# Kernel tuning notes

Measured on AMD Instinct MI355X. Metric: run time of the kernel, lower is better.

## Reference

```python
import jax, jax.numpy as jnp
import numpy as np

H, D = 4, 32  # num_heads, per-head out dim (out_feats=128)
N_AGENT, N_GT, N_UAV = 50000, 50000, 50000
E = 600000
IN = 64


def _gat(x_src, x_dst, src, dst, W_src, W_dst, al, ar, W_res, b, num_dst):
    """DGL-style bipartite GATConv with residual, bias and ReLU activation."""
    fs = (x_src @ W_src).reshape(-1, H, D)      # [Ns,H,D]
    fd = (x_dst @ W_dst).reshape(-1, H, D)      # [Nd,H,D]
    el = jnp.sum(fs * al, axis=-1)              # [Ns,H]
    er = jnp.sum(fd * ar, axis=-1)              # [Nd,H]
    e = jax.nn.leaky_relu(el[src] + er[dst], 0.2)          # [E,H]
    # segment softmax over incoming edges of each dst node
    emax = jax.ops.segment_max(e, dst, num_segments=num_dst)   # [Nd,H], -inf for deg-0
    ee = jnp.exp(e - emax[dst])
    denom = jax.ops.segment_sum(ee, dst, num_segments=num_dst)
    a = ee / denom[dst]                          # [E,H]
    msg = fs[src] * a[:, :, None]                # [E,H,D]
    rst = jax.ops.segment_sum(msg, dst, num_segments=num_dst)  # [Nd,H,D]; zeros for deg-0
    res = (x_dst @ W_res).reshape(-1, H, D)      # residual projection
    out = jax.nn.relu(rst + res + b.reshape(1, H, D))
    return out.reshape(num_dst, H * D)


def setup_inputs() -> dict:
    key = jax.random.key(0)
    ks = jax.random.split(key, 20)
    s = 0.1  # weight init scale
    return {
        'x_gt': jax.random.normal(ks[0], (N_GT, IN), jnp.float32),
        'x_uav': jax.random.normal(ks[1], (N_UAV, IN), jnp.float32),
        'x_agent': jax.random.normal(ks[2], (N_AGENT, IN), jnp.float32),
        'src_gt': jax.random.randint(ks[3], (E,), 0, N_GT, jnp.int32),
        'dst_gt': jax.random.randint(ks[4], (E,), 0, N_AGENT, jnp.int32),
        'src_uav': jax.random.randint(ks[5], (E,), 0, N_UAV, jnp.int32),
        'dst_uav': jax.random.randint(ks[6], (E,), 0, N_AGENT, jnp.int32),
        'W_src_gt': s * jax.random.normal(ks[7], (IN, H * D), jnp.float32),
        'W_dst_gt': s * jax.random.normal(ks[8], (IN, H * D), jnp.float32),
        'attn_l_gt': s * jax.random.normal(ks[9], (H, D), jnp.float32),
        'attn_r_gt': s * jax.random.normal(ks[10], (H, D), jnp.float32),
        'W_res_gt': s * jax.random.normal(ks[11], (IN, H * D), jnp.float32),
        'b_gt': jnp.zeros((H * D,), jnp.float32),
        'W_src_uav': s * jax.random.normal(ks[12], (IN, H * D), jnp.float32),
        'W_dst_uav': s * jax.random.normal(ks[13], (IN, H * D), jnp.float32),
        'attn_l_uav': s * jax.random.normal(ks[14], (H, D), jnp.float32),
        'attn_r_uav': s * jax.random.normal(ks[15], (H, D), jnp.float32),
        'W_res_uav': s * jax.random.normal(ks[16], (IN, H * D), jnp.float32),
        'b_uav': jnp.zeros((H * D,), jnp.float32),
        'W_f': s * jax.random.normal(ks[17], (2 * H * D, H * D), jnp.float32),
        'b_f': jnp.zeros((H * D,), jnp.float32),
    }


def reference(x_gt, x_uav, x_agent, src_gt, dst_gt, src_uav, dst_uav,
              W_src_gt, W_dst_gt, attn_l_gt, attn_r_gt, W_res_gt, b_gt,
              W_src_uav, W_dst_uav, attn_l_uav, attn_r_uav, W_res_uav, b_uav,
              W_f, b_f):
    h_gt = _gat(x_gt, x_agent, src_gt, dst_gt, W_src_gt, W_dst_gt,
                attn_l_gt, attn_r_gt, W_res_gt, b_gt, N_AGENT)
    h_uav = _gat(x_uav, x_agent, src_uav, dst_uav, W_src_uav, W_dst_uav,
                 attn_l_uav, attn_r_uav, W_res_uav, b_uav, N_AGENT)
    h = jnp.concatenate([h_gt, h_uav], axis=1)   # [N_agent, 256]
    return jax.nn.relu(h @ W_f + b_f)            # [N_agent, 128]
```

## Files before the change

kernel.cpp:

```cpp
#include <hip/hip_runtime.h>
#include <hip/hip_bf16.h>

using bf16 = __hip_bfloat16;

#define NA 50000
#define NE 600000

#define NCH 96
#define CHE 12500
#define HROW 100032
#define PBINS 33344

typedef __attribute__((ext_vector_type(8))) short short8;
typedef __attribute__((ext_vector_type(4))) float f32x4;

#define HBUF_B   0u
#define FS_B     25600000u
#define EL_B     51200000u
#define RECS_B   54400000u
#define HIST_B   68800000u
#define ROW_B    78403072u
#define TOPS_B   78803076u
#define FLAG_B   78803588u
#define WST_GT_B 78803600u
#define WST_UAV_B 78819984u
#define WRT_B    78836368u
#define WFT_B    78869136u
#define ELT_GT_B 78934672u
#define ELT_UAV_B 78936720u
#define ERT_B    78938768u
#define RANK8_B  78940816u
#define WS_BYTES 80140816u

__device__ __forceinline__ float b2f(bf16 v) { return __bfloat162float(v); }

__device__ __forceinline__ float ldf(const void* p, size_t i, int f32) {
    return f32 ? ((const float*)p)[i] : b2f(((const bf16*)p)[i]);
}

__device__ __forceinline__ unsigned short f2bs(float v) {
    bf16 t = __float2bfloat16(v);
    return *(unsigned short*)&t;
}

__device__ __forceinline__ float lrelu_exp(float v) {
    v = v > 0.f ? v : 0.2f * v;
    return __expf(v);
}

__device__ __forceinline__ unsigned int pack_bf16x2(float a, float b) {
    return (unsigned int)f2bs(a) | ((unsigned int)f2bs(b) << 16);
}

__device__ __forceinline__ float lo_f(unsigned int u) { return __uint_as_float(u << 16); }
__device__ __forceinline__ float hi_f(unsigned int u) { return __uint_as_float(u & 0xffff0000u); }

__device__ __forceinline__ short8 ldfrag8(const void* p, size_t off, int f32) {
    if (!f32) return *(const short8*)((const unsigned short*)p + off);
    union { short8 s; unsigned int u[4]; } r;
    const float* fp = (const float*)p + off;
#pragma unroll
    for (int j = 0; j < 4; ++j) r.u[j] = pack_bf16x2(fp[2 * j], fp[2 * j + 1]);
    return r.s;
}

__device__ int probe_f32(const void* x0) {
    __shared__ int cnt;
    if (threadIdx.x == 0) cnt = 0;
    __syncthreads();
    const bf16* p = (const bf16*)x0;
    int bad = 0;
    for (int i = threadIdx.x; i < 1024; i += 256) {
        float av = fabsf(b2f(p[i]));
        if (!(av <= 1e6f)) bad++;
    }
    if (bad) atomicAdd(&cnt, bad);
    __syncthreads();
    return cnt > 8;
}

__global__ void HeteroVisionConv_29703993819529_kernel(
    const void* x0,
    const void* Wsg, const void* alg, const void* Wdg, const void* arg_,
    const void* Wsu, const void* alu, const void* Wdu, const void* aru,
    const void* Wrg, const void* Wru, const void* Wf,
    unsigned short* wsT_gt, unsigned short* wsT_uav, unsigned short* wrT,
    unsigned short* wfT, unsigned short* elT_gt, unsigned short* elT_uav,
    unsigned short* erT,
    int* flag, unsigned int* outp, long sent) {
    int b = blockIdx.x, t = threadIdx.x;
    int f32 = probe_f32(x0);
    if (b == 20) {
        if (t == 0) { flag[0] = f32; outp[sent] = 0x447A447Au; }
        return;
    }
    if (b < 8) {
        for (int i = t; i < 16 * 256; i += 256) {
            int n = b * 16 + (i >> 8), k = i & 255;
            wfT[n * 256 + k] = f2bs(ldf(Wf, (size_t)k * 128 + n, f32));
        }
    } else if (b < 12) {
        for (int i = t; i < 64 * 64; i += 256) {
            int n = (b - 8) * 64 + (i >> 6), k = i & 63;
            float v = (n < 128) ? ldf(Wrg, (size_t)k * 128 + n, f32)
                                : ldf(Wru, (size_t)k * 128 + (n - 128), f32);
            wrT[n * 64 + k] = f2bs(v);
        }
    } else if (b < 14) {
        for (int i = t; i < 64 * 64; i += 256) {
            int n = (b - 12) * 64 + (i >> 6), k = i & 63;
            wsT_gt[n * 64 + k] = f2bs(ldf(Wsg, (size_t)k * 128 + n, f32));
        }
    } else if (b < 16) {
        for (int i = t; i < 64 * 64; i += 256) {
            int n = (b - 14) * 64 + (i >> 6), k = i & 63;
            wsT_uav[n * 64 + k] = f2bs(ldf(Wsu, (size_t)k * 128 + n, f32));
        }
    } else {
        int m = b - 16;
        const void* Wm = (m == 0) ? Wsg : (m == 1) ? Wdg : (m == 2) ? Wsu : Wdu;
        const void* Am = (m == 0) ? alg : (m == 1) ? arg_ : (m == 2) ? alu : aru;
        int k = t >> 2, h = t & 3;
        float a = 0.f;
        for (int d = 0; d < 32; ++d)
            a += ldf(Wm, (size_t)k * 128 + h * 32 + d, f32) *
                 ldf(Am, (size_t)h * 32 + d, f32);
        unsigned short v = f2bs(a);
        if (m == 0) {
            elT_gt[h * 64 + k] = v;
            for (int i = t; i < 12 * 64; i += 256) elT_gt[(4 + (i >> 6)) * 64 + (i & 63)] = 0;
        } else if (m == 2) {
            elT_uav[h * 64 + k] = v;
            for (int i = t; i < 12 * 64; i += 256) elT_uav[(4 + (i >> 6)) * 64 + (i & 63)] = 0;
        } else if (m == 1) {
            erT[h * 64 + k] = v;
        } else {
            erT[(4 + h) * 64 + k] = v;
            for (int i = t; i < 8 * 64; i += 256) erT[(8 + (i >> 6)) * 64 + (i & 63)] = 0;
        }
    }
}

__global__ void fused_k(const int* dg, const int* du,
                        unsigned char* hist, unsigned char* rank8,
                        const void* xg, const void* xu, const void* xa,
                        const unsigned short* wsT_gt, const unsigned short* wsT_uav,
                        const unsigned short* elT_gt, const unsigned short* elT_uav,
                        const unsigned short* wrT, const unsigned short* erT,
                        const void* bg, const void* bu,
                        float* elbase, bf16* fs, bf16* hbuf, const int* flag) {
    __shared__ unsigned short Bt[256 * 72];
    __shared__ float bl[256];
    int b = blockIdx.x, t = threadIdx.x;

    if (b < NCH) {
        int c = b;
        int g = c >= 48;
        int eoff = (c - g * 48) * CHE;
        const int* dp = (g ? du : dg) + eoff;
        unsigned char* rk = rank8 + (size_t)g * NE + eoff;
        unsigned int* h32 = (unsigned int*)Bt;
        for (int p = 0; p < 3; ++p) {
            int binLo = p * PBINS;
            unsigned int* out = (unsigned int*)(hist + (size_t)c * HROW + binLo);
            bool live = (binLo + PBINS > g * NA) && (binLo < g * NA + NA);
            if (!live) {
                for (int i = t; i < PBINS / 4; i += 256) out[i] = 0u;
                continue;
            }
            for (int i = t; i < PBINS / 4; i += 256) h32[i] = 0u;
            __syncthreads();
            for (int i = t; i < CHE / 4; i += 256) {
                int4 d4 = *(const int4*)(dp + i * 4);
                int dd[4] = {d4.x, d4.y, d4.z, d4.w};
#pragma unroll
                for (int k = 0; k < 4; ++k) {
                    int rel = g * NA + dd[k] - binLo;
                    if (rel >= 0 && rel < PBINS) {
                        unsigned int sh8 = 8u * (rel & 3);
                        unsigned int old = atomicAdd(&h32[rel >> 2], 1u << sh8);
                        rk[i * 4 + k] = (unsigned char)((old >> sh8) & 255u);
                    }
                }
            }
            __syncthreads();
            for (int i = t; i < PBINS / 4; i += 256) out[i] = h32[i];
            __syncthreads();
        }
        return;
    }
    int nidx = b - NCH;
    int f32 = *flag;
    int lane = t & 63, w = t >> 6;
    int m = lane & 15, quad = lane >> 4;

    if (nidx < 1564) {
        int g = nidx / 782, bb = nidx % 782;
        const void* A = g ? xu : xg;
        const unsigned short* WT = g ? wsT_uav : wsT_gt;
        const unsigned short* ET = g ? elT_uav : elT_gt;
        float* elout = elbase + (g ? 400000 : 0);
        bf16* out = fs + (size_t)g * NA * 128;
        for (int i = t * 8; i < 128 * 64; i += 256 * 8) {
            short8 v = *(const short8*)(WT + i);
            int n = i >> 6, k = i & 63;
            *(short8*)&Bt[n * 72 + k] = v;
        }
        __syncthreads();
        int row = bb * 64 + w * 16 + m;
        int rowc = row < NA ? row : NA - 1;
        short8 a0 = ldfrag8(A, (size_t)rowc * 64 + quad * 8, f32);
        short8 a1 = ldfrag8(A, (size_t)rowc * 64 + 32 + quad * 8, f32);
        f32x4 acc[8];
#pragma unroll
        for (int nt = 0; nt < 8; ++nt) acc[nt] = (f32x4){0.f, 0.f, 0.f, 0.f};
#pragma unroll
        for (int nt = 0; nt < 8; ++nt) {
            short8 b0 = *(const short8*)&Bt[(nt * 16 + m) * 72 + quad * 8];
            short8 b1 = *(const short8*)&Bt[(nt * 16 + m) * 72 + 32 + quad * 8];
            acc[nt] = __builtin_amdgcn_mfma_f32_16x16x32_bf16(a0, b0, acc[nt], 0, 0, 0);
            acc[nt] = __builtin_amdgcn_mfma_f32_16x16x32_bf16(a1, b1, acc[nt], 0, 0, 0);
        }
        f32x4 eacc = (f32x4){0.f, 0.f, 0.f, 0.f};
        {
            short8 e0 = *(const short8*)&ET[m * 64 + quad * 8];
            short8 e1 = *(const short8*)&ET[m * 64 + 32 + quad * 8];
            eacc = __builtin_amdgcn_mfma_f32_16x16x32_bf16(a0, e0, eacc, 0, 0, 0);
            eacc = __builtin_amdgcn_mfma_f32_16x16x32_bf16(a1, e1, eacc, 0, 0, 0);
        }
        int srow = bb * 64 + w * 16 + quad * 4;
#pragma unroll
        for (int nt = 0; nt < 8; ++nt) {
#pragma unroll
            for (int r = 0; r < 4; ++r) {
                int rr = srow + r;
                if (rr < NA) out[(size_t)rr * 128 + nt * 16 + m] = __float2bfloat16(acc[nt][r]);
            }
        }
        if (m < 4) {
#pragma unroll
            for (int r = 0; r < 4; ++r) {
                int rr = srow + r;
                if (rr < NA) elout[(size_t)rr * 4 + m] = eacc[r];
            }
        }
        return;
    }
    int bb = nidx - 1564;
    for (int i = t * 8; i < 256 * 64; i += 256 * 8) {
        short8 v = *(const short8*)(wrT + i);
        int n = i >> 6, k = i & 63;
        *(short8*)&Bt[n * 72 + k] = v;
    }
    bl[t] = (t < 128) ? ldf(bg, t, f32) : ldf(bu, t - 128, f32);
    __syncthreads();
    int row = bb * 64 + w * 16 + m;
    int rowc = row < NA ? row : NA - 1;
    short8 a0 = ldfrag8(xa, (size_t)rowc * 64 + quad * 8, f32);
    short8 a1 = ldfrag8(xa, (size_t)rowc * 64 + 32 + quad * 8, f32);
    f32x4 acc[16];
#pragma unroll
    for (int nt = 0; nt < 16; ++nt) acc[nt] = (f32x4){0.f, 0.f, 0.f, 0.f};
#pragma unroll
    for (int nt = 0; nt < 16; ++nt) {
        short8 b0 = *(const short8*)&Bt[(nt * 16 + m) * 72 + quad * 8];
        short8 b1 = *(const short8*)&Bt[(nt * 16 + m) * 72 + 32 + quad * 8];
        acc[nt] = __builtin_amdgcn_mfma_f32_16x16x32_bf16(a0, b0, acc[nt], 0, 0, 0);
        acc[nt] = __builtin_amdgcn_mfma_f32_16x16x32_bf16(a1, b1, acc[nt], 0, 0, 0);
    }
    f32x4 eacc = (f32x4){0.f, 0.f, 0.f, 0.f};
    {
        short8 e0 = *(const short8*)&erT[m * 64 + quad * 8];
        short8 e1 = *(const short8*)&erT[m * 64 + 32 + quad * 8];
        eacc = __builtin_amdgcn_mfma_f32_16x16x32_bf16(a0, e0, eacc, 0, 0, 0);
        eacc = __builtin_amdgcn_mfma_f32_16x16x32_bf16(a1, e1, eacc, 0, 0, 0);
    }
    int srow = bb * 64 + w * 16 + quad * 4;
#pragma unroll
    for (int nt = 0; nt < 16; ++nt) {
        int col = nt * 16 + m;
#pragma unroll
        for (int r = 0; r < 4; ++r) {
            int rr = srow + r;
            if (rr < NA)
                hbuf[(size_t)rr * 256 + col] = __float2bfloat16(acc[nt][r] + bl[col]);
        }
    }
    if (m < 8) {
        float* ero = (m < 4) ? (elbase + 200000) : (elbase + 600000);
        int mm = m & 3;
#pragma unroll
        for (int r = 0; r < 4; ++r) {
            int rr = srow + r;
            if (rr < NA) ero[(size_t)rr * 4 + mm] = eacc[r];
        }
    }
}

__global__ void scan1_k(unsigned char* hist, unsigned int* row, unsigned int* tops) {
    __shared__ unsigned char ch[NCH * 1024];
    __shared__ unsigned int sh[256];
    int b = blockIdx.x, t = threadIdx.x;
    int base = b * 1024;
    int off = base + t * 4;
    for (int c = 0; c < NCH; ++c) {
        unsigned int w = 0u;
        if (off + 4 <= HROW) w = *(const unsigned int*)(hist + (size_t)c * HROW + off);
        *(unsigned int*)&ch[c * 1024 + t * 4] = w;
    }
    __syncthreads();
    unsigned int v[4];
    for (int j = 0; j < 4; ++j) {
        int idx = t * 4 + j;
        unsigned int run = 0;
        for (int c = 0; c < NCH; ++c) {
            unsigned int x = ch[c * 1024 + idx];
            ch[c * 1024 + idx] = (unsigned char)run;
            run += x;
        }
        v[j] = (base + idx < 100000) ? run : 0u;
    }
    __syncthreads();
    for (int c = 0; c < NCH; ++c) {
        if (off + 4 <= HROW)
            *(unsigned int*)(hist + (size_t)c * HROW + off) =
                *(const unsigned int*)&ch[c * 1024 + t * 4];
    }
    unsigned int s = v[0] + v[1] + v[2] + v[3];
    sh[t] = s;
    __syncthreads();
    for (int o = 1; o < 256; o <<= 1) {
        unsigned int x = (t >= o) ? sh[t - o] : 0u;
        __syncthreads();
        sh[t] += x;
        __syncthreads();
    }
    unsigned int run = sh[t] - s;
    for (int j = 0; j < 4; ++j) {
        if (base + j + t * 4 < 100000) row[base + t * 4 + j] = run;
        run += v[j];
    }
    if (t == 255) tops[b] = sh[255];
}

__global__ void scan2_k(unsigned int* tops, unsigned int* row) {
    __shared__ unsigned int sh[128];
    int t = threadIdx.x;
    unsigned int v = (t < 98) ? tops[t] : 0u;
    sh[t] = v;
    __syncthreads();
    for (int off = 1; off < 128; off <<= 1) {
        unsigned int x = (t >= off) ? sh[t - off] : 0u;
        __syncthreads();
        sh[t] += x;
        __syncthreads();
    }
    if (t < 98) tops[t] = sh[t] - v;
    if (t == 97) row[100000] = sh[97];
}

__global__ void scan3_k(unsigned int* row, const unsigned int* tops) {
    int b = blockIdx.x, t = threadIdx.x;
    unsigned int off = tops[b];
    for (int i = b * 1024 + t; i < b * 1024 + 1024; i += 256) {
        if (i < 100000) row[i] += off;
    }
}

__global__ void scatter_k(const int* sg, const int* dg, const int* su, const int* du,
                          const float* elbase, const unsigned int* row,
                          const unsigned char* hist, const unsigned char* rank8,
                          unsigned int* recs) {
    int idx = blockIdx.x * 256 + threadIdx.x;
    if (idx >= 2 * NE) return;
    int g = idx >= NE;
    int e = idx - g * NE;
    int s = (g ? su : sg)[e];
    int d = (g ? du : dg)[e];
    int c = g * 48 + e / CHE;
    int bin = g * NA + d;
    const float4* el4 = (const float4*)(elbase + (g ? 400000 : 0));
    const float4* er4 = (const float4*)(elbase + (g ? 600000 : 200000));
    unsigned int lr = rank8[idx];
    unsigned int cb = hist[(size_t)c * HROW + bin];
    unsigned int pos = row[bin] + cb + lr;
    float4 l = el4[s], r = er4[d];
    uint3 rec;
    rec.x = (unsigned int)s;
    rec.y = pack_bf16x2(lrelu_exp(l.x + r.x), lrelu_exp(l.y + r.y));
    rec.z = pack_bf16x2(lrelu_exp(l.z + r.z), lrelu_exp(l.w + r.w));
    *(uint3*)(recs + (size_t)pos * 3) = rec;
}

__global__ void gather_k(const unsigned int* row, const unsigned int* recs,
                         const bf16* fs, bf16* hbuf) {
    int wid = (blockIdx.x * 256 + threadIdx.x) >> 6;
    int lane = threadIdx.x & 63;
    if (wid >= 2 * NA) return;
    int g = wid / NA, d = wid - g * NA;
    int eg = lane >> 4;
    int cl = lane & 15;
    int hsel = cl >> 3;
    int hodd = (cl >> 2) & 1;
    unsigned int start = row[g * NA + d];
    unsigned int end   = row[g * NA + d + 1];
    const uint4* fs4 = (const uint4*)(fs + (size_t)g * NA * 128);

    float denom = 0.f;
    float a[8];
#pragma unroll
    for (int k = 0; k < 8; ++k) a[k] = 0.f;

    if (start < end) {
        uint3 rr[4], rn[4];
#pragma unroll
        for (int j = 0; j < 4; ++j) {
            unsigned int idx = start + 4 * j + eg;
            rr[j] = *(const uint3*)(recs + (size_t)(idx < end ? idx : end - 1) * 3);
        }
        for (unsigned int i = start; i < end; i += 16) {
            uint4 uu[4];
#pragma unroll
            for (int j = 0; j < 4; ++j) uu[j] = fs4[(size_t)rr[j].x * 16 + cl];
            unsigned int inext = i + 16;
#pragma unroll
            for (int j = 0; j < 4; ++j) {
                unsigned int idx = inext + 4 * j + eg;
                rn[j] = *(const uint3*)(recs + (size_t)(idx < end ? idx : end - 1) * 3);
            }
#pragma unroll
            for (int j = 0; j < 4; ++j) {
                unsigned int idx = i + 4 * j + eg;
                unsigned int pp = hsel ? rr[j].z : rr[j].y;
                float e = hodd ? hi_f(pp) : lo_f(pp);
                if (idx >= end) e = 0.f;
                denom += e;
                a[0] += lo_f(uu[j].x) * e;
                a[1] += hi_f(uu[j].x) * e;
                a[2] += lo_f(uu[j].y) * e;
                a[3] += hi_f(uu[j].y) * e;
                a[4] += lo_f(uu[j].z) * e;
                a[5] += hi_f(uu[j].z) * e;
                a[6] += lo_f(uu[j].w) * e;
                a[7] += hi_f(uu[j].w) * e;
            }
#pragma unroll
            for (int j = 0; j < 4; ++j) rr[j] = rn[j];
        }
    }
#pragma unroll
    for (int k = 0; k < 8; ++k) {
        a[k] += __shfl_xor(a[k], 16, 64);
        a[k] += __shfl_xor(a[k], 32, 64);
    }
    denom += __shfl_xor(denom, 16, 64);
    denom += __shfl_xor(denom, 32, 64);
    if (lane < 16) {
        float inv = (end > start) ? 1.f / denom : 0.f;
        uint4* hp = (uint4*)(hbuf + (size_t)d * 256 + g * 128) + cl;
        uint4 rv = *hp;
        float v0 = a[0] * inv + lo_f(rv.x);
        float v1 = a[1] * inv + hi_f(rv.x);
        float v2 = a[2] * inv + lo_f(rv.y);
        float v3 = a[3] * inv + hi_f(rv.y);
        float v4 = a[4] * inv + lo_f(rv.z);
        float v5 = a[5] * inv + hi_f(rv.z);
        float v6 = a[6] * inv + lo_f(rv.w);
        float v7 = a[7] * inv + hi_f(rv.w);
        v0 = v0 > 0.f ? v0 : 0.f;
        v1 = v1 > 0.f ? v1 : 0.f;
        v2 = v2 > 0.f ? v2 : 0.f;
        v3 = v3 > 0.f ? v3 : 0.f;
        v4 = v4 > 0.f ? v4 : 0.f;
        v5 = v5 > 0.f ? v5 : 0.f;
        v6 = v6 > 0.f ? v6 : 0.f;
        v7 = v7 > 0.f ? v7 : 0.f;
        uint4 o;
        o.x = pack_bf16x2(v0, v1);
        o.y = pack_bf16x2(v2, v3);
        o.z = pack_bf16x2(v4, v5);
        o.w = pack_bf16x2(v6, v7);
        *hp = o;
    }
}

__global__ void final_k(const bf16* hbuf, const unsigned short* wfT,
                        const void* bfp, void* outp, const int* flag) {
    int f32 = *flag;
    int b = blockIdx.x;
    __shared__ unsigned short Bt[128 * 72];
    __shared__ float bl[128];
    int t = threadIdx.x;
    if (t < 128) bl[t] = ldf(bfp, t, f32);
    int lane = t & 63, w = t >> 6;
    int m = lane & 15, quad = lane >> 4;
    int row = b * 64 + w * 16 + m;
    int rowc = row < NA ? row : NA - 1;
    f32x4 acc[8];
#pragma unroll
    for (int nt = 0; nt < 8; ++nt) acc[nt] = (f32x4){0.f, 0.f, 0.f, 0.f};
    for (int kc = 0; kc < 4; ++kc) {
        __syncthreads();
        for (int i = t * 8; i < 128 * 64; i += 256 * 8) {
            int n = i >> 6, k = i & 63;
            short8 v = *(const short8*)(wfT + (size_t)n * 256 + kc * 64 + k);
            *(short8*)&Bt[n * 72 + k] = v;
        }
        __syncthreads();
        short8 a0 = *(const short8*)((const unsigned short*)hbuf +
                                     (size_t)rowc * 256 + kc * 64 + quad * 8);
        short8 a1 = *(const short8*)((const unsigned short*)hbuf +
                                     (size_t)rowc * 256 + kc * 64 + 32 + quad * 8);
#pragma unroll
        for (int nt = 0; nt < 8; ++nt) {
            short8 b0 = *(const short8*)&Bt[(nt * 16 + m) * 72 + quad * 8];
            short8 b1 = *(const short8*)&Bt[(nt * 16 + m) * 72 + 32 + quad * 8];
            acc[nt] = __builtin_amdgcn_mfma_f32_16x16x32_bf16(a0, b0, acc[nt], 0, 0, 0);
            acc[nt] = __builtin_amdgcn_mfma_f32_16x16x32_bf16(a1, b1, acc[nt], 0, 0, 0);
        }
    }
    int srow = b * 64 + w * 16 + quad * 4;
#pragma unroll
    for (int nt = 0; nt < 8; ++nt) {
        int col = nt * 16 + m;
        float bv = bl[col];
#pragma unroll
        for (int r = 0; r < 4; ++r) {
            int rr = srow + r;
            if (rr < NA) {
                float v = acc[nt][r] + bv;
                v = v > 0.f ? v : 0.f;
                if (f32) ((float*)outp)[(size_t)rr * 128 + col] = v;
                else ((bf16*)outp)[(size_t)rr * 128 + col] = __float2bfloat16(v);
            }
        }
    }
}

extern "C" void kernel_launch(void* const* d_in, const int* in_sizes, int n_in,
                              void* d_out, int out_size, void* d_ws, size_t ws_size,
                              hipStream_t stream) {
    const void* x_gt     = d_in[0];
    const void* x_uav    = d_in[1];
    const void* x_ag     = d_in[2];
    const int*  src_gt   = (const int*)d_in[3];
    const int*  dst_gt   = (const int*)d_in[4];
    const int*  src_uav  = (const int*)d_in[5];
    const int*  dst_uav  = (const int*)d_in[6];
    const void* Wsrc_gt  = d_in[7];
    const void* Wdst_gt  = d_in[8];
    const void* al_gt    = d_in[9];
    const void* ar_gt    = d_in[10];
    const void* Wres_gt  = d_in[11];
    const void* b_gt     = d_in[12];
    const void* Wsrc_uav = d_in[13];
    const void* Wdst_uav = d_in[14];
    const void* al_uav   = d_in[15];
    const void* ar_uav   = d_in[16];
    const void* Wres_uav = d_in[17];
    const void* b_uav    = d_in[18];
    const void* W_f      = d_in[19];
    const void* b_f      = d_in[20];

    char* wsb = (char*)d_ws;
    bf16* hbuf = (bf16*)(wsb + HBUF_B);
    bf16* fs = (bf16*)(wsb + FS_B);
    float* el = (float*)(wsb + EL_B);
    unsigned int* recs = (unsigned int*)(wsb + RECS_B);
    unsigned char* hist = (unsigned char*)(wsb + HIST_B);
    unsigned int* row = (unsigned int*)(wsb + ROW_B);
    unsigned int* tops = (unsigned int*)(wsb + TOPS_B);
    int* flag = (int*)(wsb + FLAG_B);
    unsigned short* wsT_gt = (unsigned short*)(wsb + WST_GT_B);
    unsigned short* wsT_uav = (unsigned short*)(wsb + WST_UAV_B);
    unsigned short* wrT = (unsigned short*)(wsb + WRT_B);
    unsigned short* wfT = (unsigned short*)(wsb + WFT_B);
    unsigned short* elT_gt = (unsigned short*)(wsb + ELT_GT_B);
    unsigned short* elT_uav = (unsigned short*)(wsb + ELT_UAV_B);
    unsigned short* erT = (unsigned short*)(wsb + ERT_B);
    unsigned char* rank8 = (unsigned char*)(wsb + RANK8_B);

    if (ws_size < (size_t)WS_BYTES) {
        hipMemsetAsync(d_out, 0x42, (size_t)out_size * 2, stream);
        return;
    }

    long sent = (long)out_size / 2 - 1;

    HeteroVisionConv_29703993819529_kernel<<<21, 256, 0, stream>>>(
        x_gt, Wsrc_gt, al_gt, Wdst_gt, ar_gt, Wsrc_uav, al_uav, Wdst_uav, ar_uav,
        Wres_gt, Wres_uav, W_f,
        wsT_gt, wsT_uav, wrT, wfT, elT_gt, elT_uav, erT,
        flag, (unsigned int*)d_out, sent);
    fused_k<<<NCH + 2346, 256, 0, stream>>>(dst_gt, dst_uav, hist, rank8,
                                            x_gt, x_uav, x_ag,
                                            wsT_gt, wsT_uav, elT_gt, elT_uav,
                                            wrT, erT, b_gt, b_uav,
                                            el, fs, hbuf, flag);
    scan1_k<<<98, 256, 0, stream>>>(hist, row, tops);
    scan2_k<<<1, 128, 0, stream>>>(tops, row);
    scan3_k<<<98, 256, 0, stream>>>(row, tops);
    scatter_k<<<4688, 256, 0, stream>>>(src_gt, dst_gt, src_uav, dst_uav,
                                        el, row, hist, rank8, recs);
    gather_k<<<25000, 256, 0, stream>>>(row, recs, fs, hbuf);
    final_k<<<782, 256, 0, stream>>>(hbuf, wfT, b_f, d_out, flag);
}
```

Before: 302.2 us.

## Fold scan passes into last-block decoupled scan and pipeline gather loop

The three-kernel prefix scan becomes one kernel. The last block to finish, found with an atomic ticket counter, scans the per-block totals, and consumers add the block offset on read instead of running a separate fixup pass. This removes two kernel launches and a full pass over the row array. The gather loop is also restructured from 16-edge batches with 4 records per lane to a 4-edge-per-step software pipeline that prefetches two records ahead, and bf16 extraction now uses a shift instead of a select. The trade-offs are an extra tops load per scatter and per gather, and a different memory-level parallelism profile in gather.

```diff
diff --git a/kernel.cpp b/kernel.cpp
--- a/kernel.cpp
+++ b/kernel.cpp
@@ -86,12 +86,12 @@
     const void* Wrg, const void* Wru, const void* Wf,
     unsigned short* wsT_gt, unsigned short* wsT_uav, unsigned short* wrT,
     unsigned short* wfT, unsigned short* elT_gt, unsigned short* elT_uav,
-    unsigned short* erT,
+    unsigned short* erT, unsigned int* tops,
     int* flag, unsigned int* outp, long sent) {
     int b = blockIdx.x, t = threadIdx.x;
     int f32 = probe_f32(x0);
     if (b == 20) {
-        if (t == 0) { flag[0] = f32; outp[sent] = 0x447A447Au; }
+        if (t == 0) { flag[0] = f32; tops[120] = 0u; outp[sent] = 0x447A447Au; }
         return;
     }
     if (b < 8) {
@@ -300,6 +300,7 @@
 __global__ void scan1_k(unsigned char* hist, unsigned int* row, unsigned int* tops) {
     __shared__ unsigned char ch[NCH * 1024];
     __shared__ unsigned int sh[256];
+    __shared__ int lastf;
     int b = blockIdx.x, t = threadIdx.x;
     int base = b * 1024;
     int off = base + t * 4;
@@ -337,38 +338,37 @@
     }
     unsigned int run = sh[t] - s;
     for (int j = 0; j < 4; ++j) {
-        if (base + j + t * 4 < 100000) row[base + t * 4 + j] = run;
+        if (base + t * 4 + j < 100000) row[base + t * 4 + j] = run;
         run += v[j];
     }
     if (t == 255) tops[b] = sh[255];
-}
-
-__global__ void scan2_k(unsigned int* tops, unsigned int* row) {
-    __shared__ unsigned int sh[128];
-    int t = threadIdx.x;
-    unsigned int v = (t < 98) ? tops[t] : 0u;
-    sh[t] = v;
-    __syncthreads();
-    for (int off = 1; off < 128; off <<= 1) {
-        unsigned int x = (t >= off) ? sh[t - off] : 0u;
+    __threadfence();
+    __syncthreads();
+    if (t == 0) {
+        unsigned int tk = atomicAdd(&tops[120], 1u);
+        lastf = (tk == 97u);
+    }
+    __syncthreads();
+    if (!lastf) return;
+    unsigned int tv = (t < 98) ? __hip_atomic_load(&tops[t], __ATOMIC_RELAXED,
+                                                   __HIP_MEMORY_SCOPE_AGENT)
+                               : 0u;
+    __syncthreads();
+    sh[t] = tv;
+    __syncthreads();
+    for (int o = 1; o < 256; o <<= 1) {
+        unsigned int x = (t >= o) ? sh[t - o] : 0u;
         __syncthreads();
         sh[t] += x;
         __syncthreads();
     }
-    if (t < 98) tops[t] = sh[t] - v;
-    if (t == 97) row[100000] = sh[97];
-}
-
-__global__ void scan3_k(unsigned int* row, const unsigned int* tops) {
-    int b = blockIdx.x, t = threadIdx.x;
-    unsigned int off = tops[b];
-    for (int i = b * 1024 + t; i < b * 1024 + 1024; i += 256) {
-        if (i < 100000) row[i] += off;
-    }
+    if (t < 98) tops[t] = sh[t] - tv;
+    if (t == 97) row[100000] = tv;
 }
 
 __global__ void scatter_k(const int* sg, const int* dg, const int* su, const int* du,
                           const float* elbase, const unsigned int* row,
+                          const unsigned int* tops,
                           const unsigned char* hist, const unsigned char* rank8,
                           unsigned int* recs) {
     int idx = blockIdx.x * 256 + threadIdx.x;
@@ -383,7 +383,7 @@
     const float4* er4 = (const float4*)(elbase + (g ? 600000 : 200000));
     unsigned int lr = rank8[idx];
     unsigned int cb = hist[(size_t)c * HROW + bin];
-    unsigned int pos = row[bin] + cb + lr;
+    unsigned int pos = row[bin] + tops[bin >> 10] + cb + lr;
     float4 l = el4[s], r = er4[d];
     uint3 rec;
     rec.x = (unsigned int)s;
@@ -392,18 +392,20 @@
     *(uint3*)(recs + (size_t)pos * 3) = rec;
 }
 
-__global__ void gather_k(const unsigned int* row, const unsigned int* recs,
+__global__ void gather_k(const unsigned int* row, const unsigned int* tops,
+                         const unsigned int* recs,
                          const bf16* fs, bf16* hbuf) {
     int wid = (blockIdx.x * 256 + threadIdx.x) >> 6;
     int lane = threadIdx.x & 63;
     if (wid >= 2 * NA) return;
     int g = wid / NA, d = wid - g * NA;
+    int bin = g * NA + d;
     int eg = lane >> 4;
     int cl = lane & 15;
     int hsel = cl >> 3;
-    int hodd = (cl >> 2) & 1;
-    unsigned int start = row[g * NA + d];
-    unsigned int end   = row[g * NA + d + 1];
+    unsigned int shl = ((cl >> 2) & 1) ? 0u : 16u;
+    unsigned int start = row[bin] + tops[bin >> 10];
+    unsigned int end   = row[bin + 1] + tops[(bin + 1) >> 10];
     const uint4* fs4 = (const uint4*)(fs + (size_t)g * NA * 128);
 
     float denom = 0.f;
@@ -412,40 +414,28 @@
     for (int k = 0; k < 8; ++k) a[k] = 0.f;
 
     if (start < end) {
-        uint3 rr[4], rn[4];
-#pragma unroll
-        for (int j = 0; j < 4; ++j) {
-            unsigned int idx = start + 4 * j + eg;
-            rr[j] = *(const uint3*)(recs + (size_t)(idx < end ? idx : end - 1) * 3);
-        }
-        for (unsigned int i = start; i < end; i += 16) {
-            uint4 uu[4];
-#pragma unroll
-            for (int j = 0; j < 4; ++j) uu[j] = fs4[(size_t)rr[j].x * 16 + cl];
-            unsigned int inext = i + 16;
-#pragma unroll
-            for (int j = 0; j < 4; ++j) {
-                unsigned int idx = inext + 4 * j + eg;
-                rn[j] = *(const uint3*)(recs + (size_t)(idx < end ? idx : end - 1) * 3);
-            }
-#pragma unroll
-            for (int j = 0; j < 4; ++j) {
-                unsigned int idx = i + 4 * j + eg;
-                unsigned int pp = hsel ? rr[j].z : rr[j].y;
-                float e = hodd ? hi_f(pp) : lo_f(pp);
-                if (idx >= end) e = 0.f;
-                denom += e;
-                a[0] += lo_f(uu[j].x) * e;
-                a[1] += hi_f(uu[j].x) * e;
-                a[2] += lo_f(uu[j].y) * e;
-                a[3] += hi_f(uu[j].y) * e;
-                a[4] += lo_f(uu[j].z) * e;
-                a[5] += hi_f(uu[j].z) * e;
-                a[6] += lo_f(uu[j].w) * e;
-                a[7] += hi_f(uu[j].w) * e;
-            }
-#pragma unroll
-            for (int j = 0; j < 4; ++j) rr[j] = rn[j];
+        unsigned int i0 = start + eg;
+        uint3 rc = *(const uint3*)(recs + (size_t)(i0 < end ? i0 : end - 1) * 3);
+        uint4 u = fs4[(size_t)rc.x * 16 + cl];
+        unsigned int i1 = start + 4 + eg;
+        uint3 rn = *(const uint3*)(recs + (size_t)(i1 < end ? i1 : end - 1) * 3);
+        for (unsigned int i = start; i < end; i += 4) {
+            uint4 un = fs4[(size_t)rn.x * 16 + cl];
+            unsigned int i2 = i + 8 + eg;
+            uint3 rnn = *(const uint3*)(recs + (size_t)(i2 < end ? i2 : end - 1) * 3);
+            unsigned int pp = hsel ? rc.z : rc.y;
+            float e = __uint_as_float((pp << shl) & 0xffff0000u);
+            if (i + eg >= end) e = 0.f;
+            denom += e;
+            a[0] += lo_f(u.x) * e;
+            a[1] += hi_f(u.x) * e;
+            a[2] += lo_f(u.y) * e;
+            a[3] += hi_f(u.y) * e;
+            a[4] += lo_f(u.z) * e;
+            a[5] += hi_f(u.z) * e;
+            a[6] += lo_f(u.w) * e;
+            a[7] += hi_f(u.w) * e;
+            rc = rn; rn = rnn; u = un;
         }
     }
 #pragma unroll
@@ -590,7 +580,7 @@
     HeteroVisionConv_29703993819529_kernel<<<21, 256, 0, stream>>>(
         x_gt, Wsrc_gt, al_gt, Wdst_gt, ar_gt, Wsrc_uav, al_uav, Wdst_uav, ar_uav,
         Wres_gt, Wres_uav, W_f,
-        wsT_gt, wsT_uav, wrT, wfT, elT_gt, elT_uav, erT,
+        wsT_gt, wsT_uav, wrT, wfT, elT_gt, elT_uav, erT, tops,
         flag, (unsigned int*)d_out, sent);
     fused_k<<<NCH + 2346, 256, 0, stream>>>(dst_gt, dst_uav, hist, rank8,
                                             x_gt, x_uav, x_ag,
@@ -598,10 +588,8 @@
                                             wrT, erT, b_gt, b_uav,
                                             el, fs, hbuf, flag);
     scan1_k<<<98, 256, 0, stream>>>(hist, row, tops);
-    scan2_k<<<1, 128, 0, stream>>>(tops, row);
-    scan3_k<<<98, 256, 0, stream>>>(row, tops);
     scatter_k<<<4688, 256, 0, stream>>>(src_gt, dst_gt, src_uav, dst_uav,
-                                        el, row, hist, rank8, recs);
-    gather_k<<<25000, 256, 0, stream>>>(row, recs, fs, hbuf);
+                                        el, row, tops, hist, rank8, recs);
+    gather_k<<<25000, 256, 0, stream>>>(row, tops, recs, fs, hbuf);
     final_k<<<782, 256, 0, stream>>>(hbuf, wfT, b_f, d_out, flag);
 }
```

After: 311.3 us. 3.0% more time.
